# Optimization experiments

Measured on AMD Instinct MI355X. Metric: run time of the kernel, lower is better.

The kernel has to match this reference:

```python
import jax, jax.numpy as jnp
import numpy as np

V, E, H, L, MAXLEN, B = 32000, 512, 512, 2, 99, 4096

def setup_inputs() -> dict:
    key = jax.random.key(0)
    ks = jax.random.split(key, 16)
    s = 0.02
    return {
        "inputs": jax.random.randint(ks[0], (B, 1), 0, V),
        "hidden": jax.random.normal(ks[1], (L, B, H), dtype=jnp.float32),
        "encoder_outputs": jax.random.normal(ks[2], (B, MAXLEN, H), dtype=jnp.float32),
        "embedding": jax.random.normal(ks[3], (V, E), dtype=jnp.float32) * s,
        "attn_W": jax.random.normal(ks[4], (MAXLEN, 2 * H), dtype=jnp.float32) * s,
        "attn_b": jnp.zeros((MAXLEN,), jnp.float32),
        "combine_W": jax.random.normal(ks[5], (H, 2 * H), dtype=jnp.float32) * s,
        "combine_b": jnp.zeros((H,), jnp.float32),
        "W_ih": jax.random.normal(ks[6], (L, 3 * H, H), dtype=jnp.float32) * s,
        "W_hh": jax.random.normal(ks[7], (L, 3 * H, H), dtype=jnp.float32) * s,
        "b_ih": jnp.zeros((L, 3 * H), jnp.float32),
        "b_hh": jnp.zeros((L, 3 * H), jnp.float32),
        "out_W": jax.random.normal(ks[8], (V, H), dtype=jnp.float32) * s,
        "out_b": jnp.zeros((V,), jnp.float32),
    }

def reference(inputs, hidden, encoder_outputs, embedding, attn_W, attn_b,
              combine_W, combine_b, W_ih, W_hh, b_ih, b_hh, out_W, out_b):
    # embedding lookup (dropout is identity in eval)
    emb = embedding[inputs[:, 0]]                                   # [B, E]
    # Bahdanau-style attention over encoder outputs
    q = jnp.concatenate([emb, hidden[0]], axis=1)                   # [B, 2H]
    attn_weights = jax.nn.softmax(q @ attn_W.T + attn_b, axis=1)    # [B, max_len]
    attn_applied = jnp.einsum('bl,blh->bh', attn_weights, encoder_outputs)  # [B, H]
    x = jax.nn.relu(jnp.concatenate([emb, attn_applied], axis=1) @ combine_W.T + combine_b)  # [B, H]
    # single-step multi-layer GRU (PyTorch gate math)
    n_layers = hidden.shape[0]
    new_h = []
    inp = x
    for l in range(n_layers):  # small fixed structural loop
        h = hidden[l]
        gi = inp @ W_ih[l].T + b_ih[l]
        gh = h @ W_hh[l].T + b_hh[l]
        i_r, i_z, i_n = jnp.split(gi, 3, axis=1)
        h_r, h_z, h_n = jnp.split(gh, 3, axis=1)
        r = jax.nn.sigmoid(i_r + h_r)
        z = jax.nn.sigmoid(i_z + h_z)
        n = jnp.tanh(i_n + r * h_n)
        h_new = (1.0 - z) * n + z * h
        new_h.append(h_new)
        inp = h_new
    hidden_new = jnp.stack(new_h)                                   # [L, B, H]
    pred = jax.nn.softmax(inp @ out_W.T + out_b, axis=1)            # [B, V]
    return pred, hidden_new, attn_weights
```

## Files before the change

kernel.cpp:

```cpp
#include <hip/hip_runtime.h>
#include <cstdint>
#include <cstddef>
#include <cmath>

#define B 4096
#define H 512
#define E 512
#define V 32000
#define NL 2
#define MAXLEN 99

typedef __attribute__((ext_vector_type(8))) short  bf16x8;
typedef __attribute__((ext_vector_type(4))) float  f32x4;
typedef __attribute__((ext_vector_type(8))) unsigned short ushort8;

__device__ __forceinline__ unsigned short f2b(float x) {
    union { float f; unsigned u; } c; c.f = x;
    unsigned r = c.u + 0x7fff + ((c.u >> 16) & 1);
    return (unsigned short)(r >> 16);
}
__device__ __forceinline__ float b2f(unsigned short u) {
    return __uint_as_float((unsigned)u << 16);
}

#define GLOAD16(gp, lp)                                                        \
    __builtin_amdgcn_global_load_lds(                                          \
        (const __attribute__((address_space(1))) void*)(gp),                   \
        (__attribute__((address_space(3))) void*)(lp), 16, 0, 0)

__global__ __launch_bounds__(256) void embed_concat_kernel(
    const int* __restrict__ tok, const float* __restrict__ emb,
    const float* __restrict__ hidden0, float* __restrict__ q, float* __restrict__ c2)
{
    const int b = blockIdx.x, t = threadIdx.x;
    const int v = tok[b];
    const float2 e = ((const float2*)(emb + (size_t)v * E))[t];
    ((float2*)(q  + (size_t)b * 1024))[t] = e;
    ((float2*)(c2 + (size_t)b * 1024))[t] = e;
    const float2 h = ((const float2*)(hidden0 + (size_t)b * H))[t];
    ((float2*)(q + (size_t)b * 1024 + 512))[t] = h;
}

__global__ __launch_bounds__(256) void attn_fused_kernel(
    const float* __restrict__ q, const float* __restrict__ attn_W,
    const float* __restrict__ attn_b, const float* __restrict__ enc,
    float* __restrict__ attnw, float* __restrict__ c2)
{
    const int b = blockIdx.x, t = threadIdx.x;
    __shared__ float qs[1024];
    __shared__ float ls[128];

    ((float4*)qs)[t] = ((const float4*)(q + (size_t)b * 1024))[t];
    __syncthreads();

    float s = -1e30f;
    if (t < MAXLEN) {
        const float4* w4 = (const float4*)(attn_W + (size_t)t * 1024);
        const float4* q4 = (const float4*)qs;
        float ax = 0.f, ay = 0.f, az = 0.f, aw = 0.f;
        #pragma unroll 8
        for (int k = 0; k < 256; ++k) {
            const float4 a = q4[k], w = w4[k];
            ax += a.x * w.x; ay += a.y * w.y; az += a.z * w.z; aw += a.w * w.w;
        }
        s = (ax + ay) + (az + aw) + attn_b[t];
    }
    if (t < 128) ls[t] = s;
    __syncthreads();

    float mx = -1e30f;
    for (int i = 0; i < 128; ++i) mx = fmaxf(mx, ls[i]);
    __syncthreads();

    float ex = 0.f;
    if (t < MAXLEN) ex = expf(s - mx);
    if (t < 128) ls[t] = ex;
    __syncthreads();

    float sum = 0.f;
    for (int i = 0; i < 128; ++i) sum += ls[i];
    const float inv = 1.0f / sum;

    if (t < MAXLEN) attnw[(size_t)b * MAXLEN + t] = ex * inv;

    float accx = 0.f, accy = 0.f;
    const float2* encb = (const float2*)(enc + (size_t)b * MAXLEN * H);
    for (int l = 0; l < MAXLEN; ++l) {
        const float wl = ls[l];
        const float2 ev = encb[(size_t)l * 256 + t];
        accx += wl * ev.x; accy += wl * ev.y;
    }
    float2 outv; outv.x = accx * inv; outv.y = accy * inv;
    ((float2*)(c2 + (size_t)b * 1024 + 512))[t] = outv;
}

__global__ __launch_bounds__(256) void f32_to_bf16_kernel(
    const float* __restrict__ in, unsigned short* __restrict__ out)
{
    const size_t i = ((size_t)blockIdx.x * 256 + threadIdx.x) * 8;
    const float4 a = *(const float4*)(in + i);
    const float4 b = *(const float4*)(in + i + 4);
    ushort8 o;
    o[0] = f2b(a.x); o[1] = f2b(a.y); o[2] = f2b(a.z); o[3] = f2b(a.w);
    o[4] = f2b(b.x); o[5] = f2b(b.y); o[6] = f2b(b.z); o[7] = f2b(b.w);
    *(ushort8*)(out + i) = o;
}

template<int RELU, int OUTBF, int PARTIALS, int GSWAP>
__global__ __launch_bounds__(256) void gemm_bf16_nt(
    const unsigned short* __restrict__ A, const unsigned short* __restrict__ Wb,
    const float* __restrict__ bias, void* __restrict__ Cv,
    int M, int N, int K, int ldc, int colOff,
    float* __restrict__ pmax_g, float* __restrict__ psum_g)
{
    __shared__ __align__(16) unsigned short As[2][4096];
    __shared__ __align__(16) unsigned short Bs[2][4096];

    const int tid  = threadIdx.x;
    const int bn   = (GSWAP ? blockIdx.y : blockIdx.x) * 128;
    const int bm   = (GSWAP ? blockIdx.x : blockIdx.y) * 128;
    const int lane = tid & 63;
    const int wid  = tid >> 6;
    const int wr   = (wid >> 1) * 64;
    const int wc   = (wid & 1) * 64;
    const int fr   = lane & 15;
    const int fk   = (lane >> 4) * 8;

    f32x4 acc[4][4];
    #pragma unroll
    for (int m = 0; m < 4; ++m)
        #pragma unroll
        for (int n = 0; n < 4; ++n) acc[m][n] = (f32x4)0.f;

    const int srow = tid >> 2;
    const int sk   = (tid & 3) * 8;

    const unsigned short* ga = A  + (size_t)(bm + srow) * K + sk;
    const unsigned short* gb = Wb + (size_t)(bn + srow) * K + sk;

    {
        GLOAD16(ga,                    &As[0][tid * 8]);
        GLOAD16(ga + (size_t)64 * K,   &As[0][2048 + tid * 8]);
        GLOAD16(gb,                    &Bs[0][tid * 8]);
        GLOAD16(gb + (size_t)64 * K,   &Bs[0][2048 + tid * 8]);
    }

    int buf = 0;
    for (int k0 = 0; k0 < K; k0 += 32) {
        __syncthreads();

        if (k0 + 32 < K) {
            const int nb = buf ^ 1;
            GLOAD16(ga + k0 + 32,                  &As[nb][tid * 8]);
            GLOAD16(ga + k0 + 32 + (size_t)64 * K, &As[nb][2048 + tid * 8]);
            GLOAD16(gb + k0 + 32,                  &Bs[nb][tid * 8]);
            GLOAD16(gb + k0 + 32 + (size_t)64 * K, &Bs[nb][2048 + tid * 8]);
        }

        bf16x8 af[4], bf_[4];
        #pragma unroll
        for (int m = 0; m < 4; ++m)
            af[m] = *(const bf16x8*)&As[buf][(wr + m * 16 + fr) * 32 + fk];
        #pragma unroll
        for (int n = 0; n < 4; ++n)
            bf_[n] = *(const bf16x8*)&Bs[buf][(wc + n * 16 + fr) * 32 + fk];

        #pragma unroll
        for (int m = 0; m < 4; ++m)
            #pragma unroll
            for (int n = 0; n < 4; ++n)
                acc[m][n] = __builtin_amdgcn_mfma_f32_16x16x32_bf16(
                    af[m], bf_[n], acc[m][n], 0, 0, 0);

        buf ^= 1;
    }

    float bv[4];
    #pragma unroll
    for (int n = 0; n < 4; ++n) bv[n] = bias[bn + wc + n * 16 + fr];

    if constexpr (PARTIALS) {
        __shared__ float pm_s[2][2][64];
        __shared__ float ps_s[2][2][64];
        const int wrIdx = wid >> 1, wcIdx = wid & 1;

        #pragma unroll
        for (int m = 0; m < 4; ++m) {
            #pragma unroll
            for (int r = 0; r < 4; ++r) {
                float vmax = -1e30f;
                #pragma unroll
                for (int n = 0; n < 4; ++n) vmax = fmaxf(vmax, acc[m][n][r] + bv[n]);
                vmax = fmaxf(vmax, __shfl_xor(vmax, 1));
                vmax = fmaxf(vmax, __shfl_xor(vmax, 2));
                vmax = fmaxf(vmax, __shfl_xor(vmax, 4));
                vmax = fmaxf(vmax, __shfl_xor(vmax, 8));
                float vsum = 0.f;
                #pragma unroll
                for (int n = 0; n < 4; ++n) vsum += expf(acc[m][n][r] + bv[n] - vmax);
                vsum += __shfl_xor(vsum, 1);
                vsum += __shfl_xor(vsum, 2);
                vsum += __shfl_xor(vsum, 4);
                vsum += __shfl_xor(vsum, 8);
                const int rowh = m * 16 + (lane >> 4) * 4 + r;
                if (fr == 0) { pm_s[wrIdx][wcIdx][rowh] = vmax; ps_s[wrIdx][wcIdx][rowh] = vsum; }
            }
        }
        __syncthreads();
        if (wcIdx == 0) {
            const float m0 = pm_s[wrIdx][0][lane], m1 = pm_s[wrIdx][1][lane];
            const float s0 = ps_s[wrIdx][0][lane], s1 = ps_s[wrIdx][1][lane];
            const float Mx = fmaxf(m0, m1);
            const float S  = s0 * expf(m0 - Mx) + s1 * expf(m1 - Mx);
            const int row = bm + wr + lane;
            const int nt  = bn >> 7;
            const int NT  = N >> 7;
            pmax_g[(size_t)row * NT + nt] = Mx;
            psum_g[(size_t)row * NT + nt] = S;
        }
    }

    if constexpr (OUTBF) {
        __syncthreads();
        unsigned short* smb = (wr == 0) ? (unsigned short*)As : (unsigned short*)Bs;
        #pragma unroll
        for (int m = 0; m < 4; ++m) {
            #pragma unroll
            for (int n = 0; n < 4; ++n) {
                #pragma unroll
                for (int r = 0; r < 4; ++r) {
                    float v = acc[m][n][r] + bv[n];
                    if (RELU) v = fmaxf(v, 0.f);
                    const int row  = m * 16 + (lane >> 4) * 4 + r;
                    const int col  = wc + n * 16 + fr;
                    const int cc   = col ^ ((row & 12) << 3);
                    smb[row * 128 + cc] = f2b(v);
                }
            }
        }
        __syncthreads();
        unsigned short* Cb = (unsigned short*)Cv;
        const int rrow = tid >> 4;
        const int cch  = (tid & 15) * 8;
        #pragma unroll
        for (int p = 0; p < 8; ++p) {
            const int row  = p * 16 + rrow;
            const int lrow = row & 63;
            unsigned short* smr = (p < 4) ? (unsigned short*)As : (unsigned short*)Bs;
            const int cc = cch ^ ((row & 12) << 3);
            const ushort8 v = *(const ushort8*)&smr[lrow * 128 + cc];
            *(ushort8*)&Cb[(size_t)(bm + row) * ldc + colOff + bn + cch] = v;
        }
    } else {
        float* Cf = (float*)Cv;
        #pragma unroll
        for (int m = 0; m < 4; ++m) {
            #pragma unroll
            for (int n = 0; n < 4; ++n) {
                const int col = bn + wc + n * 16 + fr;
                const int row = bm + wr + m * 16 + (lane >> 4) * 4;
                #pragma unroll
                for (int r = 0; r < 4; ++r) {
                    float v = acc[m][n][r] + bv[n];
                    if (RELU) v = fmaxf(v, 0.f);
                    Cf[(size_t)(row + r) * ldc + colOff + col] = v;
                }
            }
        }
    }
}

template<int RELU>
__global__ __launch_bounds__(256) void gemm_nt(
    const float* __restrict__ A, const float* __restrict__ W,
    const float* __restrict__ bias, float* __restrict__ C,
    int M, int N, int K)
{
    constexpr int BM = 128, BN = 128, BK = 32;
    __shared__ float As[BK][BM + 4];
    __shared__ float Bs[BK][BN + 4];

    const int tid = threadIdx.x;
    const int bn = blockIdx.x * BN;
    const int bm = blockIdx.y * BM;
    const int tx = tid & 15;
    const int ty = tid >> 4;

    float acc[8][8];
    #pragma unroll
    for (int i = 0; i < 8; ++i)
        #pragma unroll
        for (int j = 0; j < 8; ++j) acc[i][j] = 0.f;

    const int lkv = tid & 7;
    const int lm0 = tid >> 3;

    for (int k0 = 0; k0 < K; k0 += BK) {
        #pragma unroll
        for (int r = 0; r < 4; ++r) {
            const int m = lm0 + 32 * r;
            const float4 va = *(const float4*)(A + (size_t)(bm + m) * K + k0 + lkv * 4);
            As[lkv * 4 + 0][m] = va.x; As[lkv * 4 + 1][m] = va.y;
            As[lkv * 4 + 2][m] = va.z; As[lkv * 4 + 3][m] = va.w;
            const float4 vb = *(const float4*)(W + (size_t)(bn + m) * K + k0 + lkv * 4);
            Bs[lkv * 4 + 0][m] = vb.x; Bs[lkv * 4 + 1][m] = vb.y;
            Bs[lkv * 4 + 2][m] = vb.z; Bs[lkv * 4 + 3][m] = vb.w;
        }
        __syncthreads();

        #pragma unroll
        for (int kk = 0; kk < BK; ++kk) {
            float a[8], bb[8];
            *(float4*)&a[0]  = *(const float4*)&As[kk][ty * 8];
            *(float4*)&a[4]  = *(const float4*)&As[kk][ty * 8 + 4];
            *(float4*)&bb[0] = *(const float4*)&Bs[kk][tx * 8];
            *(float4*)&bb[4] = *(const float4*)&Bs[kk][tx * 8 + 4];
            #pragma unroll
            for (int i = 0; i < 8; ++i)
                #pragma unroll
                for (int j = 0; j < 8; ++j) acc[i][j] += a[i] * bb[j];
        }
        __syncthreads();
    }

    #pragma unroll
    for (int i = 0; i < 8; ++i) {
        const int row = bm + ty * 8 + i;
        float* crow = C + (size_t)row * N + bn + tx * 8;
        #pragma unroll
        for (int j = 0; j < 8; ++j) {
            float v = acc[i][j] + bias[bn + tx * 8 + j];
            if (RELU) v = fmaxf(v, 0.f);
            crow[j] = v;
        }
    }
}

__global__ __launch_bounds__(256) void gru_gates_kernel(
    const unsigned short* __restrict__ gi, const unsigned short* __restrict__ gh,
    const float* __restrict__ h, float* __restrict__ hnew,
    unsigned short* __restrict__ hnew_b)
{
    const int i = blockIdx.x * 256 + threadIdx.x;
    const int b = i >> 9, j = i & 511;
    const size_t base = (size_t)b * 1536;
    const float ir = b2f(gi[base + j]), iz = b2f(gi[base + 512 + j]), in_ = b2f(gi[base + 1024 + j]);
    const float hr = b2f(gh[base + j]), hz = b2f(gh[base + 512 + j]), hn  = b2f(gh[base + 1024 + j]);
    const float r = 1.f / (1.f + expf(-(ir + hr)));
    const float z = 1.f / (1.f + expf(-(iz + hz)));
    const float n = tanhf(in_ + r * hn);
    const float hv = (1.f - z) * n + z * h[i];
    hnew[i] = hv;
    hnew_b[i] = f2b(hv);
}

__global__ __launch_bounds__(64) void softmax_rowstats_kernel(
    const float* __restrict__ pmax, const float* __restrict__ psum,
    float* __restrict__ rowM, float* __restrict__ rowInvS, int NT)
{
    const int row = blockIdx.x, t = threadIdx.x;
    float Mx = -1e30f, S = 0.f;
    for (int i = t; i < NT; i += 64) {
        const float m = pmax[(size_t)row * NT + i];
        const float s = psum[(size_t)row * NT + i];
        const float nm = fmaxf(Mx, m);
        S = S * expf(Mx - nm) + s * expf(m - nm);
        Mx = nm;
    }
    #pragma unroll
    for (int mask = 1; mask < 64; mask <<= 1) {
        const float m2 = __shfl_xor(Mx, mask);
        const float s2 = __shfl_xor(S, mask);
        const float nm = fmaxf(Mx, m2);
        S = S * expf(Mx - nm) + s2 * expf(m2 - nm);
        Mx = nm;
    }
    if (t == 0) { rowM[row] = Mx; rowInvS[row] = 1.f / S; }
}

__global__ __launch_bounds__(256) void softmax_apply_tophalf_kernel(
    float* logits, const float* __restrict__ rowM,
    const float* __restrict__ rowInvS)
{
    const int row = blockIdx.x, t = threadIdx.x;
    const float Mx = rowM[row], is = rowInvS[row];
    const unsigned short* src = (const unsigned short*)logits + (size_t)row * (2 * V) + V;
    ushort8 buf[16];
    #pragma unroll
    for (int k = 0; k < 16; ++k) {
        const int i = t + 256 * k;
        if (i < V / 8) buf[k] = *(const ushort8*)&src[i * 8];
    }
    __syncthreads();
    float* dst = logits + (size_t)row * V;
    #pragma unroll
    for (int k = 0; k < 16; ++k) {
        const int i = t + 256 * k;
        if (i < V / 8) {
            float4 o0, o1;
            o0.x = expf(b2f(buf[k][0]) - Mx) * is;
            o0.y = expf(b2f(buf[k][1]) - Mx) * is;
            o0.z = expf(b2f(buf[k][2]) - Mx) * is;
            o0.w = expf(b2f(buf[k][3]) - Mx) * is;
            o1.x = expf(b2f(buf[k][4]) - Mx) * is;
            o1.y = expf(b2f(buf[k][5]) - Mx) * is;
            o1.z = expf(b2f(buf[k][6]) - Mx) * is;
            o1.w = expf(b2f(buf[k][7]) - Mx) * is;
            *(float4*)&dst[i * 8]     = o0;
            *(float4*)&dst[i * 8 + 4] = o1;
        }
    }
}

__global__ __launch_bounds__(256) void softmax_rows_kernel(float* __restrict__ logits, int N)
{
    const int b = blockIdx.x, t = threadIdx.x;
    __shared__ float red[256];
    float* row = logits + (size_t)b * N;

    float mx = -1e30f;
    for (int i = t; i < N; i += 256) mx = fmaxf(mx, row[i]);
    red[t] = mx; __syncthreads();
    for (int s = 128; s > 0; s >>= 1) { if (t < s) red[t] = fmaxf(red[t], red[t + s]); __syncthreads(); }
    mx = red[0]; __syncthreads();

    float sum = 0.f;
    for (int i = t; i < N; i += 256) sum += expf(row[i] - mx);
    red[t] = sum; __syncthreads();
    for (int s = 128; s > 0; s >>= 1) { if (t < s) red[t] += red[t + s]; __syncthreads(); }
    const float inv = 1.0f / red[0];
    __syncthreads();

    for (int i = t; i < N; i += 256) row[i] = expf(row[i] - mx) * inv;
}

extern "C" void kernel_launch(void* const* d_in, const int* in_sizes, int n_in,
                              void* d_out, int out_size, void* d_ws, size_t ws_size,
                              hipStream_t stream)
{
    const int*   tok    = (const int*)d_in[0];
    const float* hidden = (const float*)d_in[1];
    const float* enc    = (const float*)d_in[2];
    const float* emb    = (const float*)d_in[3];
    const float* attn_W = (const float*)d_in[4];
    const float* attn_b = (const float*)d_in[5];
    const float* comb_W = (const float*)d_in[6];
    const float* comb_b = (const float*)d_in[7];
    const float* W_ih   = (const float*)d_in[8];
    const float* W_hh   = (const float*)d_in[9];
    const float* b_ih   = (const float*)d_in[10];
    const float* b_hh   = (const float*)d_in[11];
    const float* out_W  = (const float*)d_in[12];
    const float* out_b  = (const float*)d_in[13];

    float* out   = (float*)d_out;
    float* pred  = out;
    float* hid_o = out + (size_t)B * V;
    float* attnw = hid_o + (size_t)NL * B * H;

    float* q  = pred;
    float* c2 = q  + (size_t)B * 1024;

    unsigned short* sb     = (unsigned short*)(c2 + (size_t)B * 1024);
    unsigned short* c2b    = sb;
    unsigned short* xb     = c2b  + (size_t)B * 1024;
    unsigned short* h01b   = xb   + (size_t)B * 512;
    unsigned short* hn0b   = h01b + (size_t)NL * B * 512;
    unsigned short* gi_b   = hn0b + (size_t)B * 512;
    unsigned short* gh_b   = gi_b + (size_t)B * 1536;
    unsigned short* Wihb   = gh_b + (size_t)B * 1536;
    unsigned short* Whhb   = Wihb + (size_t)NL * 1536 * 512;
    unsigned short* combWb = Whhb + (size_t)NL * 1536 * 512;
    unsigned short* hn1b_fallback = combWb + (size_t)512 * 1024;

    const size_t outWb_e = (size_t)V * H;
    const size_t hn1b_e  = (size_t)B * H;
    const int    NT      = V / 128;
    const size_t bf_bytes = (outWb_e + hn1b_e) * sizeof(unsigned short);
    const size_t pt_bytes = ((size_t)B * NT * 2 + 2 * B) * sizeof(float);
    const bool lvl1 = ws_size >= bf_bytes;
    const bool lvl2 = ws_size >= bf_bytes + pt_bytes;

    unsigned short* outWb = (unsigned short*)d_ws;
    unsigned short* hn1b  = lvl1 ? outWb + outWb_e : hn1b_fallback;
    float* pmax_g  = (float*)((char*)d_ws + bf_bytes);
    float* psum_g  = pmax_g + (size_t)B * NT;
    float* rowM    = psum_g + (size_t)B * NT;
    float* rowInvS = rowM + B;

    unsigned short* h0b = h01b;
    unsigned short* h1b = h01b + (size_t)B * 512;

    embed_concat_kernel<<<B, 256, 0, stream>>>(tok, emb, hidden, q, c2);
    attn_fused_kernel<<<B, 256, 0, stream>>>(q, attn_W, attn_b, enc, attnw, c2);

    f32_to_bf16_kernel<<<(B * 1024) / 2048, 256, 0, stream>>>(c2, c2b);
    f32_to_bf16_kernel<<<(512 * 1024) / 2048, 256, 0, stream>>>(comb_W, combWb);
    f32_to_bf16_kernel<<<(NL * 1536 * 512) / 2048, 256, 0, stream>>>(W_ih, Wihb);
    f32_to_bf16_kernel<<<(NL * 1536 * 512) / 2048, 256, 0, stream>>>(W_hh, Whhb);
    f32_to_bf16_kernel<<<(NL * B * 512) / 2048, 256, 0, stream>>>(hidden, h01b);
    if (lvl1)
        f32_to_bf16_kernel<<<(V * 512) / 2048, 256, 0, stream>>>(out_W, outWb);

    gemm_bf16_nt<1, 1, 0, 0><<<dim3(512 / 128, B / 128), 256, 0, stream>>>(
        c2b, combWb, comb_b, xb, B, 512, 1024, 512, 0, nullptr, nullptr);

    gemm_bf16_nt<0, 1, 0, 0><<<dim3(1536 / 128, B / 128), 256, 0, stream>>>(
        xb, Wihb, b_ih, gi_b, B, 1536, 512, 1536, 0, nullptr, nullptr);
    gemm_bf16_nt<0, 1, 0, 0><<<dim3(1536 / 128, B / 128), 256, 0, stream>>>(
        h0b, Whhb, b_hh, gh_b, B, 1536, 512, 1536, 0, nullptr, nullptr);
    gru_gates_kernel<<<(B * H) / 256, 256, 0, stream>>>(gi_b, gh_b, hidden, hid_o, hn0b);

    gemm_bf16_nt<0, 1, 0, 0><<<dim3(1536 / 128, B / 128), 256, 0, stream>>>(
        hn0b, Wihb + (size_t)1536 * 512, b_ih + 1536, gi_b, B, 1536, 512, 1536, 0, nullptr, nullptr);
    gemm_bf16_nt<0, 1, 0, 0><<<dim3(1536 / 128, B / 128), 256, 0, stream>>>(
        h1b, Whhb + (size_t)1536 * 512, b_hh + 1536, gh_b, B, 1536, 512, 1536, 0, nullptr, nullptr);
    gru_gates_kernel<<<(B * H) / 256, 256, 0, stream>>>(
        gi_b, gh_b, hidden + (size_t)B * H, hid_o + (size_t)B * H, hn1b);

    if (lvl2) {
        gemm_bf16_nt<0, 1, 1, 1><<<dim3(B / 128, V / 128), 256, 0, stream>>>(
            hn1b, outWb, out_b, pred, B, V, 512, 2 * V, V, pmax_g, psum_g);
        softmax_rowstats_kernel<<<B, 64, 0, stream>>>(pmax_g, psum_g, rowM, rowInvS, NT);
        softmax_apply_tophalf_kernel<<<B, 256, 0, stream>>>(pred, rowM, rowInvS);
    } else if (lvl1) {
        gemm_bf16_nt<0, 0, 0, 1><<<dim3(B / 128, V / 128), 256, 0, stream>>>(
            hn1b, outWb, out_b, pred, B, V, 512, V, 0, nullptr, nullptr);
        softmax_rows_kernel<<<B, 256, 0, stream>>>(pred, V);
    } else {
        gemm_nt<0><<<dim3(V / 128, B / 128), 256, 0, stream>>>(
            hid_o + (size_t)B * H, out_W, out_b, pred, B, V, 512);
        softmax_rows_kernel<<<B, 256, 0, stream>>>(pred, V);
    }
}
```

Measured before the change: 923.8 us.

## Fuse embedding into attention, batch bf16 casts, merge GRU GEMM pairs, vectorize gates

Folds the embedding/concat kernel into the attention kernel, which now writes its bf16 combine input directly. This drops the fp32 q/c2 intermediates and one conversion pass. All weight and hidden fp32-to-bf16 conversions go into one multi-segment launch, and each GRU layer's input and hidden GEMMs become one launch with a z-dimension of two. The gate kernel now handles eight elements per thread with 16-byte vector loads and stores. These changes cut launch count and memory traffic, at the cost of branchy segment selection in the conversion kernel.

```diff
diff --git a/kernel.cpp b/kernel.cpp
--- a/kernel.cpp
+++ b/kernel.cpp
@@ -28,29 +28,23 @@
         (const __attribute__((address_space(1))) void*)(gp),                   \
         (__attribute__((address_space(3))) void*)(lp), 16, 0, 0)
 
-__global__ __launch_bounds__(256) void embed_concat_kernel(
+__global__ __launch_bounds__(256) void embed_attn_kernel(
     const int* __restrict__ tok, const float* __restrict__ emb,
-    const float* __restrict__ hidden0, float* __restrict__ q, float* __restrict__ c2)
-{
-    const int b = blockIdx.x, t = threadIdx.x;
-    const int v = tok[b];
-    const float2 e = ((const float2*)(emb + (size_t)v * E))[t];
-    ((float2*)(q  + (size_t)b * 1024))[t] = e;
-    ((float2*)(c2 + (size_t)b * 1024))[t] = e;
-    const float2 h = ((const float2*)(hidden0 + (size_t)b * H))[t];
-    ((float2*)(q + (size_t)b * 1024 + 512))[t] = h;
-}
-
-__global__ __launch_bounds__(256) void attn_fused_kernel(
-    const float* __restrict__ q, const float* __restrict__ attn_W,
+    const float* __restrict__ hidden0, const float* __restrict__ attn_W,
     const float* __restrict__ attn_b, const float* __restrict__ enc,
-    float* __restrict__ attnw, float* __restrict__ c2)
+    float* __restrict__ attnw, unsigned short* __restrict__ c2b)
 {
     const int b = blockIdx.x, t = threadIdx.x;
     __shared__ float qs[1024];
     __shared__ float ls[128];
 
-    ((float4*)qs)[t] = ((const float4*)(q + (size_t)b * 1024))[t];
+    const int v = tok[b];
+    const float2 e = ((const float2*)(emb + (size_t)v * E))[t];
+    qs[2 * t] = e.x; qs[2 * t + 1] = e.y;
+    ushort2 eb; eb.x = f2b(e.x); eb.y = f2b(e.y);
+    *(ushort2*)&c2b[(size_t)b * 1024 + 2 * t] = eb;
+    const float2 h = ((const float2*)(hidden0 + (size_t)b * H))[t];
+    qs[512 + 2 * t] = h.x; qs[512 + 2 * t + 1] = h.y;
     __syncthreads();
 
     float s = -1e30f;
@@ -90,35 +84,44 @@
         const float2 ev = encb[(size_t)l * 256 + t];
         accx += wl * ev.x; accy += wl * ev.y;
     }
-    float2 outv; outv.x = accx * inv; outv.y = accy * inv;
-    ((float2*)(c2 + (size_t)b * 1024 + 512))[t] = outv;
-}
-
-__global__ __launch_bounds__(256) void f32_to_bf16_kernel(
-    const float* __restrict__ in, unsigned short* __restrict__ out)
-{
-    const size_t i = ((size_t)blockIdx.x * 256 + threadIdx.x) * 8;
-    const float4 a = *(const float4*)(in + i);
-    const float4 b = *(const float4*)(in + i + 4);
+    ushort2 ab; ab.x = f2b(accx * inv); ab.y = f2b(accy * inv);
+    *(ushort2*)&c2b[(size_t)b * 1024 + 512 + 2 * t] = ab;
+}
+
+__global__ __launch_bounds__(256) void batch_f2b_kernel(
+    const float* __restrict__ s0, unsigned short* __restrict__ d0, int e0,
+    const float* __restrict__ s1, unsigned short* __restrict__ d1, int e1,
+    const float* __restrict__ s2, unsigned short* __restrict__ d2, int e2,
+    const float* __restrict__ s3, unsigned short* __restrict__ d3, int e3,
+    const float* __restrict__ s4, unsigned short* __restrict__ d4)
+{
+    int blk = blockIdx.x;
+    const float* s; unsigned short* d;
+    if      (blk < e0) { s = s0; d = d0; }
+    else if (blk < e1) { s = s1; d = d1; blk -= e0; }
+    else if (blk < e2) { s = s2; d = d2; blk -= e1; }
+    else if (blk < e3) { s = s3; d = d3; blk -= e2; }
+    else               { s = s4; d = d4; blk -= e3; }
+    const size_t i = ((size_t)blk * 256 + threadIdx.x) * 8;
+    const float4 a = *(const float4*)(s + i);
+    const float4 b = *(const float4*)(s + i + 4);
     ushort8 o;
     o[0] = f2b(a.x); o[1] = f2b(a.y); o[2] = f2b(a.z); o[3] = f2b(a.w);
     o[4] = f2b(b.x); o[5] = f2b(b.y); o[6] = f2b(b.z); o[7] = f2b(b.w);
-    *(ushort8*)(out + i) = o;
-}
-
-template<int RELU, int OUTBF, int PARTIALS, int GSWAP>
-__global__ __launch_bounds__(256) void gemm_bf16_nt(
+    *(ushort8*)(d + i) = o;
+}
+
+template<int RELU, int OUTBF, int PARTIALS>
+__device__ __forceinline__ void gemm_core(
     const unsigned short* __restrict__ A, const unsigned short* __restrict__ Wb,
     const float* __restrict__ bias, void* __restrict__ Cv,
     int M, int N, int K, int ldc, int colOff,
-    float* __restrict__ pmax_g, float* __restrict__ psum_g)
+    float* __restrict__ pmax_g, float* __restrict__ psum_g, int bm, int bn)
 {
     __shared__ __align__(16) unsigned short As[2][4096];
     __shared__ __align__(16) unsigned short Bs[2][4096];
 
     const int tid  = threadIdx.x;
-    const int bn   = (GSWAP ? blockIdx.y : blockIdx.x) * 128;
-    const int bm   = (GSWAP ? blockIdx.x : blockIdx.y) * 128;
     const int lane = tid & 63;
     const int wid  = tid >> 6;
     const int wr   = (wid >> 1) * 64;
@@ -270,6 +273,35 @@
     }
 }
 
+template<int RELU, int OUTBF, int PARTIALS, int GSWAP>
+__global__ __launch_bounds__(256) void gemm_bf16_nt(
+    const unsigned short* __restrict__ A, const unsigned short* __restrict__ Wb,
+    const float* __restrict__ bias, void* __restrict__ Cv,
+    int M, int N, int K, int ldc, int colOff,
+    float* __restrict__ pmax_g, float* __restrict__ psum_g)
+{
+    const int bn = (GSWAP ? blockIdx.y : blockIdx.x) * 128;
+    const int bm = (GSWAP ? blockIdx.x : blockIdx.y) * 128;
+    gemm_core<RELU, OUTBF, PARTIALS>(A, Wb, bias, Cv, M, N, K, ldc, colOff,
+                                     pmax_g, psum_g, bm, bn);
+}
+
+__global__ __launch_bounds__(256) void gemm_bf16_dual(
+    const unsigned short* __restrict__ A0, const unsigned short* __restrict__ W0,
+    const float* __restrict__ b0, void* __restrict__ C0,
+    const unsigned short* __restrict__ A1, const unsigned short* __restrict__ W1,
+    const float* __restrict__ b1, void* __restrict__ C1,
+    int M, int N, int K, int ldc)
+{
+    const int bn = blockIdx.x * 128;
+    const int bm = blockIdx.y * 128;
+    const unsigned short* A = blockIdx.z ? A1 : A0;
+    const unsigned short* W = blockIdx.z ? W1 : W0;
+    const float* bias       = blockIdx.z ? b1 : b0;
+    void* C                 = blockIdx.z ? C1 : C0;
+    gemm_core<0, 1, 0>(A, W, bias, C, M, N, K, ldc, 0, nullptr, nullptr, bm, bn);
+}
+
 template<int RELU>
 __global__ __launch_bounds__(256) void gemm_nt(
     const float* __restrict__ A, const float* __restrict__ W,
@@ -341,17 +373,36 @@
     const float* __restrict__ h, float* __restrict__ hnew,
     unsigned short* __restrict__ hnew_b)
 {
-    const int i = blockIdx.x * 256 + threadIdx.x;
-    const int b = i >> 9, j = i & 511;
+    const int idx = blockIdx.x * 256 + threadIdx.x;
+    const int b  = idx >> 6;
+    const int j8 = (idx & 63) * 8;
     const size_t base = (size_t)b * 1536;
-    const float ir = b2f(gi[base + j]), iz = b2f(gi[base + 512 + j]), in_ = b2f(gi[base + 1024 + j]);
-    const float hr = b2f(gh[base + j]), hz = b2f(gh[base + 512 + j]), hn  = b2f(gh[base + 1024 + j]);
-    const float r = 1.f / (1.f + expf(-(ir + hr)));
-    const float z = 1.f / (1.f + expf(-(iz + hz)));
-    const float n = tanhf(in_ + r * hn);
-    const float hv = (1.f - z) * n + z * h[i];
-    hnew[i] = hv;
-    hnew_b[i] = f2b(hv);
+    const ushort8 vir = *(const ushort8*)&gi[base + j8];
+    const ushort8 viz = *(const ushort8*)&gi[base + 512 + j8];
+    const ushort8 vin = *(const ushort8*)&gi[base + 1024 + j8];
+    const ushort8 vhr = *(const ushort8*)&gh[base + j8];
+    const ushort8 vhz = *(const ushort8*)&gh[base + 512 + j8];
+    const ushort8 vhn = *(const ushort8*)&gh[base + 1024 + j8];
+    const size_t hi = (size_t)b * 512 + j8;
+    const float4 h0 = *(const float4*)&h[hi];
+    const float4 h1 = *(const float4*)&h[hi + 4];
+    const float hval[8] = {h0.x, h0.y, h0.z, h0.w, h1.x, h1.y, h1.z, h1.w};
+    float hv[8];
+    ushort8 ob;
+    #pragma unroll
+    for (int k = 0; k < 8; ++k) {
+        const float r = 1.f / (1.f + expf(-(b2f(vir[k]) + b2f(vhr[k]))));
+        const float z = 1.f / (1.f + expf(-(b2f(viz[k]) + b2f(vhz[k]))));
+        const float n = tanhf(b2f(vin[k]) + r * b2f(vhn[k]));
+        hv[k] = (1.f - z) * n + z * hval[k];
+        ob[k] = f2b(hv[k]);
+    }
+    float4 o0, o1;
+    o0.x = hv[0]; o0.y = hv[1]; o0.z = hv[2]; o0.w = hv[3];
+    o1.x = hv[4]; o1.y = hv[5]; o1.z = hv[6]; o1.w = hv[7];
+    *(float4*)&hnew[hi]     = o0;
+    *(float4*)&hnew[hi + 4] = o1;
+    *(ushort8*)&hnew_b[hi]  = ob;
 }
 
 __global__ __launch_bounds__(64) void softmax_rowstats_kernel(
@@ -458,11 +509,7 @@
     float* hid_o = out + (size_t)B * V;
     float* attnw = hid_o + (size_t)NL * B * H;
 
-    float* q  = pred;
-    float* c2 = q  + (size_t)B * 1024;
-
-    unsigned short* sb     = (unsigned short*)(c2 + (size_t)B * 1024);
-    unsigned short* c2b    = sb;
+    unsigned short* c2b    = (unsigned short*)pred;
     unsigned short* xb     = c2b  + (size_t)B * 1024;
     unsigned short* h01b   = xb   + (size_t)B * 512;
     unsigned short* hn0b   = h01b + (size_t)NL * B * 512;
@@ -491,31 +538,33 @@
     unsigned short* h0b = h01b;
     unsigned short* h1b = h01b + (size_t)B * 512;
 
-    embed_concat_kernel<<<B, 256, 0, stream>>>(tok, emb, hidden, q, c2);
-    attn_fused_kernel<<<B, 256, 0, stream>>>(q, attn_W, attn_b, enc, attnw, c2);
-
-    f32_to_bf16_kernel<<<(B * 1024) / 2048, 256, 0, stream>>>(c2, c2b);
-    f32_to_bf16_kernel<<<(512 * 1024) / 2048, 256, 0, stream>>>(comb_W, combWb);
-    f32_to_bf16_kernel<<<(NL * 1536 * 512) / 2048, 256, 0, stream>>>(W_ih, Wihb);
-    f32_to_bf16_kernel<<<(NL * 1536 * 512) / 2048, 256, 0, stream>>>(W_hh, Whhb);
-    f32_to_bf16_kernel<<<(NL * B * 512) / 2048, 256, 0, stream>>>(hidden, h01b);
-    if (lvl1)
-        f32_to_bf16_kernel<<<(V * 512) / 2048, 256, 0, stream>>>(out_W, outWb);
+    embed_attn_kernel<<<B, 256, 0, stream>>>(
+        tok, emb, hidden, attn_W, attn_b, enc, attnw, c2b);
+
+    {
+        const int e0 = 256, e1 = e0 + 768, e2 = e1 + 768, e3 = e2 + 2048;
+        const int nblk = lvl1 ? e3 + 8000 : e3;
+        batch_f2b_kernel<<<nblk, 256, 0, stream>>>(
+            comb_W, combWb, e0,
+            W_ih,   Wihb,   e1,
+            W_hh,   Whhb,   e2,
+            hidden, h01b,   e3,
+            out_W,  outWb);
+    }
 
     gemm_bf16_nt<1, 1, 0, 0><<<dim3(512 / 128, B / 128), 256, 0, stream>>>(
         c2b, combWb, comb_b, xb, B, 512, 1024, 512, 0, nullptr, nullptr);
 
-    gemm_bf16_nt<0, 1, 0, 0><<<dim3(1536 / 128, B / 128), 256, 0, stream>>>(
-        xb, Wihb, b_ih, gi_b, B, 1536, 512, 1536, 0, nullptr, nullptr);
-    gemm_bf16_nt<0, 1, 0, 0><<<dim3(1536 / 128, B / 128), 256, 0, stream>>>(
-        h0b, Whhb, b_hh, gh_b, B, 1536, 512, 1536, 0, nullptr, nullptr);
-    gru_gates_kernel<<<(B * H) / 256, 256, 0, stream>>>(gi_b, gh_b, hidden, hid_o, hn0b);
-
-    gemm_bf16_nt<0, 1, 0, 0><<<dim3(1536 / 128, B / 128), 256, 0, stream>>>(
-        hn0b, Wihb + (size_t)1536 * 512, b_ih + 1536, gi_b, B, 1536, 512, 1536, 0, nullptr, nullptr);
-    gemm_bf16_nt<0, 1, 0, 0><<<dim3(1536 / 128, B / 128), 256, 0, stream>>>(
-        h1b, Whhb + (size_t)1536 * 512, b_hh + 1536, gh_b, B, 1536, 512, 1536, 0, nullptr, nullptr);
-    gru_gates_kernel<<<(B * H) / 256, 256, 0, stream>>>(
+    gemm_bf16_dual<<<dim3(1536 / 128, B / 128, 2), 256, 0, stream>>>(
+        xb,  Wihb, b_ih, gi_b,
+        h0b, Whhb, b_hh, gh_b, B, 1536, 512, 1536);
+    gru_gates_kernel<<<(B * H / 8) / 256, 256, 0, stream>>>(
+        gi_b, gh_b, hidden, hid_o, hn0b);
+
+    gemm_bf16_dual<<<dim3(1536 / 128, B / 128, 2), 256, 0, stream>>>(
+        hn0b, Wihb + (size_t)1536 * 512, b_ih + 1536, gi_b,
+        h1b,  Whhb + (size_t)1536 * 512, b_hh + 1536, gh_b, B, 1536, 512, 1536);
+    gru_gates_kernel<<<(B * H / 8) / 256, 256, 0, stream>>>(
         gi_b, gh_b, hidden + (size_t)B * H, hid_o + (size_t)B * H, hn1b);
 
     if (lvl2) {
```

After: 873.7 us. -5.4%, faster.
